# Optimization experiments

Measured on AMD Instinct MI355X. Metric: run time of the kernel, lower is better.

## Reference

```python
import jax, jax.numpy as jnp
import numpy as np
from jax import lax

NEG = -1e30  # safe -inf surrogate (avoids nan grads)
CTC_WEIGHT = 0.3


def _excl_cumsum(e):
    # exclusive cumsum along last axis: (..., U) -> (..., U+1)
    c = jnp.cumsum(e, axis=-1)
    return jnp.concatenate([jnp.zeros_like(c[..., :1]), c], axis=-1)


def _rnnt_loss(log_probs, targets, frame_len, tgt_len, blank):
    """RNNT forward DP. log_probs: (B,T,U+1,V) log-softmaxed. Returns per-seq NLL (B,)."""
    B, T, U1, V = log_probs.shape
    blank_lp = log_probs[..., blank]  # (B,T,U1)
    emit = jnp.take_along_axis(log_probs[:, :, :U1 - 1, :],
                               targets[:, None, :, None], axis=3)[..., 0]  # (B,T,U)
    # alpha[0,u] = sum_{j<u} emit[0,j]
    alpha0 = _excl_cumsum(emit[:, 0])  # (B,U1)

    def step(alpha_prev, inp):
        blank_prev, emit_t = inp  # (B,U1), (B,U)
        a = alpha_prev + blank_prev
        # alpha[t,u] = LSE(a_u, alpha[t,u-1] + emit[t,u-1]) solved in closed form:
        # alpha[t,u] = E[u] + cumLSE_{k<=u}(a_k - E[k]),  E = exclusive cumsum of emit
        E = _excl_cumsum(emit_t)
        alpha_t = E + lax.associative_scan(jnp.logaddexp, a - E, axis=-1)
        return alpha_t, alpha_t

    xs = (jnp.swapaxes(blank_lp[:, :-1], 0, 1), jnp.swapaxes(emit[:, 1:], 0, 1))
    _, alphas = lax.scan(step, alpha0, xs)
    alphas = jnp.concatenate([alpha0[None], alphas], axis=0)  # (T,B,U1)
    bi = jnp.arange(B)
    t_idx = frame_len - 1
    ll = alphas[t_idx, bi, tgt_len] + blank_lp[bi, t_idx, tgt_len]
    return -ll


def _ctc_loss(log_probs, targets, frame_len, tgt_len, blank):
    """CTC forward DP. log_probs: (B,T,V) log-softmaxed. Returns per-seq NLL (B,)."""
    B, T, V = log_probs.shape
    U = targets.shape[1]
    S = 2 * U + 1
    ext = jnp.full((B, S), blank, dtype=targets.dtype).at[:, 1::2].set(targets)  # (B,S)
    lp_ext = jnp.take_along_axis(log_probs, ext[:, None, :], axis=2)  # (B,T,S)
    ext_m2 = jnp.pad(ext[:, :-2], ((0, 0), (2, 0)), constant_values=blank)
    can_skip = (jnp.arange(S)[None, :] >= 2) & (ext != blank) & (ext != ext_m2)
    alpha0 = jnp.full((B, S), NEG).at[:, 0].set(lp_ext[:, 0, 0]).at[:, 1].set(lp_ext[:, 0, 1])

    def step(alpha, lp_t):
        p1 = jnp.pad(alpha[:, :-1], ((0, 0), (1, 0)), constant_values=NEG)
        p2 = jnp.where(can_skip,
                       jnp.pad(alpha[:, :-2], ((0, 0), (2, 0)), constant_values=NEG), NEG)
        m = jnp.maximum(jnp.maximum(alpha, p1), p2)
        new = lp_t + m + jnp.log(jnp.exp(alpha - m) + jnp.exp(p1 - m) + jnp.exp(p2 - m))
        return new, new

    _, alphas = lax.scan(step, alpha0, jnp.swapaxes(lp_ext, 0, 1)[1:])
    alphas = jnp.concatenate([alpha0[None], alphas], axis=0)  # (T,B,S)
    bi = jnp.arange(B)
    t_idx = frame_len - 1
    a_last = alphas[t_idx, bi, 2 * tgt_len]
    a_prev = alphas[t_idx, bi, 2 * tgt_len - 1]
    return -jnp.logaddexp(a_last, a_prev)


def setup_inputs() -> dict:
    key = jax.random.key(0)
    ks = jax.random.split(key, 9)
    B, T, U, V = 4, 200, 50, 1024
    D, H = 512, 640
    return {
        "x_enc": jax.random.normal(ks[0], (B, T, D), jnp.float32),
        "x_dec": jax.random.normal(ks[1], (B, U + 1, H), jnp.float32),
        "target": jax.random.randint(ks[2], (B, U), 0, V - 1),  # excludes blank = V-1
        "frame_length": jax.random.randint(ks[3], (B,), 150, T + 1).astype(jnp.int32),
        "target_length": jax.random.randint(ks[4], (B,), 30, U + 1).astype(jnp.int32),
        "W_ctc": jax.random.normal(ks[5], (D, V), jnp.float32) * 0.02,
        "b_ctc": jnp.zeros((V,), jnp.float32),
        "W_enc": jax.random.normal(ks[6], (D, H), jnp.float32) * 0.02,
        "W_pred": jax.random.normal(ks[7], (H, H), jnp.float32) * 0.02,
        "b_joint": jnp.zeros((H,), jnp.float32),
        "W_out": jax.random.normal(ks[8], (H, V), jnp.float32) * 0.02,
        "b_out": jnp.zeros((V,), jnp.float32),
    }


def reference(x_enc, x_dec, target, frame_length, target_length,
              W_ctc, b_ctc, W_enc, W_pred, b_joint, W_out, b_out):
    B = x_enc.shape[0]
    V = W_ctc.shape[1]
    blank = V - 1
    # CTC head: linear + log_softmax over vocab
    ctc_lp = jax.nn.log_softmax(x_enc @ W_ctc + b_ctc, axis=-1)  # (B,T,V)
    # Joiner: enc proj (B,T,1,J) + pred proj (B,1,U+1,J) -> tanh -> vocab
    joint = jnp.tanh(jnp.einsum('btd,dj->btj', x_enc, W_enc)[:, :, None, :]
                     + jnp.einsum('buh,hj->buj', x_dec, W_pred)[:, None, :, :]
                     + b_joint)  # (B,T,U+1,J)
    rnnt_lp = jax.nn.log_softmax(jnp.einsum('btuj,jv->btuv', joint, W_out) + b_out, axis=-1)
    rnnt = _rnnt_loss(rnnt_lp, target, frame_length, target_length, blank).mean()
    ctc = _ctc_loss(ctc_lp, target, frame_length, target_length, blank).sum() / B
    return rnnt + CTC_WEIGHT * ctc
```

## Files before the change

kernel.cpp:

```cpp
#include <hip/hip_runtime.h>
#include <hip/hip_bf16.h>

typedef __bf16 bf16_t;
typedef __attribute__((ext_vector_type(8))) __bf16 bf16x8;
typedef __attribute__((ext_vector_type(4))) float f32x4;
typedef __attribute__((ext_vector_type(2))) long long2_t;

#define NEGV (-1e30f)

#define BB 4
#define TT 200
#define UU 50
#define U1 51
#define VV 1024
#define DD 512
#define HH 640
#define RTOT (BB*TT*U1)
#define RPAD 40832
#define SS 101

__device__ __forceinline__ float lae(float a, float b) {
    float mx = fmaxf(a, b);
    return mx + __logf(__expf(a - mx) + __expf(b - mx));
}
__device__ __forceinline__ float lae3(float a, float b, float c) {
    float mx = fmaxf(fmaxf(a, b), c);
    return mx + __logf(__expf(a - mx) + __expf(b - mx) + __expf(c - mx));
}
__device__ __forceinline__ float tanh_fast(float x) {
    float ex = __expf(2.f * x);
    return 1.f - 2.f / (ex + 1.f);
}

__device__ __forceinline__ void pack_seg(const float* __restrict__ W, bf16_t* __restrict__ Wf,
                                         int e, int K32, int N)
{
    int j  = e & 7;
    int l  = (e >> 3) & 63;
    int kk = (e >> 9) % K32;
    int nt = e / (K32 * 512);
    int v = nt * 16 + (l & 15);
    int k = kk * 32 + ((l >> 4) << 2) + (j & 3) + ((j >> 2) << 4);
    Wf[e] = (bf16_t)W[(size_t)k * N + v];
}

__device__ __forceinline__ void pack_out8(const float* __restrict__ W, unsigned* __restrict__ Wf8,
                                          int e32)
{
    int word = e32 & 3;
    int l    = (e32 >> 2) & 63;
    int kkp  = (e32 >> 8) % 10;
    int nt   = e32 / 2560;
    int v  = nt * 16 + (l & 15);
    int kk = kkp * 2 + (word >> 1);
    int jb = (word & 1) * 4;
    float f[4];
#pragma unroll
    for (int t = 0; t < 4; ++t) {
        int j = jb + t;
        int k = kk * 32 + ((l >> 4) << 2) + (j & 3) + ((j >> 2) << 4);
        f[t] = W[(size_t)k * VV + v] * 16.f;
    }
    unsigned r = __builtin_amdgcn_cvt_pk_fp8_f32(f[0], f[1], 0, false);
    r = __builtin_amdgcn_cvt_pk_fp8_f32(f[2], f[3], r, true);
    Wf8[e32] = r;
}

__global__ void pack_all(const float* __restrict__ Wout, const float* __restrict__ Wenc,
                         const float* __restrict__ Wpred, const float* __restrict__ Wctc,
                         unsigned* __restrict__ FOut8, bf16_t* __restrict__ FEnc,
                         bf16_t* __restrict__ FPred, bf16_t* __restrict__ FCtc)
{
    int e = blockIdx.x * 256 + threadIdx.x;
    if (e < 163840) { pack_out8(Wout, FOut8, e); return; }
    e -= 163840;
    if (e < 327680) { pack_seg(Wenc, FEnc, e, 16, 640); return; }
    e -= 327680;
    if (e < 409600) { pack_seg(Wpred, FPred, e, 20, 640); return; }
    e -= 409600;
    pack_seg(Wctc, FCtc, e, 16, 1024);
}

template<int K32, int L, bool LSE, int J>
__device__ void gemm_dev(const float* __restrict__ A, int M, int rowbase, int K,
                         const bf16_t* __restrict__ Wf, const float* __restrict__ bias,
                         float* __restrict__ C, float* __restrict__ lse_out, int N,
                         bf16_t* Atile, float (*ps)[8])
{
    const int tid = threadIdx.x;
#pragma unroll
    for (int it = 0; it < J * K32 / 8; ++it) {
        int fi = it * 512 + tid;
        int l = fi & 63, jk = fi >> 6;
        int j = jk / K32, kk = jk - j * K32;
        int row = rowbase + j * 16 + (l & 15);
        if (row > M - 1) row = M - 1;
        int c0 = kk * 32 + ((l >> 4) << 2);
        const float4 a0 = *(const float4*)&A[(size_t)row * K + c0];
        const float4 a1 = *(const float4*)&A[(size_t)row * K + c0 + 16];
        bf16x8 v;
        v[0] = (bf16_t)a0.x; v[1] = (bf16_t)a0.y; v[2] = (bf16_t)a0.z; v[3] = (bf16_t)a0.w;
        v[4] = (bf16_t)a1.x; v[5] = (bf16_t)a1.y; v[6] = (bf16_t)a1.z; v[7] = (bf16_t)a1.w;
        *(bf16x8*)&Atile[(size_t)fi * 8] = v;
    }
    __syncthreads();

    const int l = tid & 63, w = tid >> 6;
    const int lrow = l & 15, lhi = l >> 4;

    f32x4 acc[J][L];
#pragma unroll
    for (int j = 0; j < J; ++j)
#pragma unroll
        for (int li = 0; li < L; ++li) acc[j][li] = f32x4{0.f, 0.f, 0.f, 0.f};

    for (int kk = 0; kk < K32; ++kk) {
        bf16x8 a[J];
#pragma unroll
        for (int j = 0; j < J; ++j)
            a[j] = *(const bf16x8*)&Atile[(size_t)(((j * K32 + kk) * 64 + l) * 8)];
#pragma unroll
        for (int li = 0; li < L; ++li) {
            bf16x8 b = *(const bf16x8*)&Wf[(size_t)(((w * L + li) * K32 + kk) * 64 + l) * 8];
#pragma unroll
            for (int j = 0; j < J; ++j)
                acc[j][li] = __builtin_amdgcn_mfma_f32_16x16x32_bf16(a[j], b, acc[j][li], 0, 0, 0);
        }
    }

    float se[J][4];
    if (LSE) {
#pragma unroll
        for (int j = 0; j < J; ++j)
#pragma unroll
            for (int i = 0; i < 4; ++i) se[j][i] = 0.f;
    }
#pragma unroll
    for (int j = 0; j < J; ++j)
#pragma unroll
        for (int li = 0; li < L; ++li) {
            int col = (w * L + li) * 16 + lrow;
            float bv = bias ? bias[col] : 0.f;
#pragma unroll
            for (int i = 0; i < 4; ++i) {
                int grow = rowbase + 16 * j + lhi * 4 + i;
                float x = acc[j][li][i] + bv;
                if (grow < M) C[(size_t)grow * N + col] = x;
                if (LSE) se[j][i] += __expf(x);
            }
        }
    if (LSE) {
#pragma unroll
        for (int d = 1; d < 16; d <<= 1)
#pragma unroll
            for (int j = 0; j < J; ++j)
#pragma unroll
                for (int i = 0; i < 4; ++i) se[j][i] += __shfl_xor(se[j][i], d);
        if (lrow == 0) {
#pragma unroll
            for (int j = 0; j < J; ++j)
#pragma unroll
                for (int i = 0; i < 4; ++i) ps[16 * j + lhi * 4 + i][w] = se[j][i];
        }
        __syncthreads();
        if (tid < J * 16) {
            float s = 0.f;
#pragma unroll
            for (int w0 = 0; w0 < 8; ++w0) s += ps[tid][w0];
            int grow = rowbase + tid;
            if (grow < M) lse_out[grow] = __logf(s);
        }
    }
}

__global__ __launch_bounds__(512)
void mfma_gemm3(const float* __restrict__ x_enc, const float* __restrict__ x_dec,
                const bf16_t* __restrict__ FEnc, const bf16_t* __restrict__ FPred,
                const bf16_t* __restrict__ FCtc, const float* __restrict__ b_ctc,
                float* __restrict__ enc_proj, float* __restrict__ pred_proj,
                float* __restrict__ ctc_logits, float* __restrict__ ctc_lse)
{
    __shared__ bf16_t Atile[40960];
    __shared__ float ps[64][8];
    int blk = blockIdx.x;
    if (blk < 13)
        gemm_dev<16, 5, false, 4>(x_enc, 800, blk * 64, 512, FEnc, nullptr, enc_proj, nullptr, 640, Atile, ps);
    else if (blk < 17)
        gemm_dev<20, 5, false, 4>(x_dec, 204, (blk - 13) * 64, 640, FPred, nullptr, pred_proj, nullptr, 640, Atile, ps);
    else
        gemm_dev<16, 8, true, 4>(x_enc, 800, (blk - 17) * 64, 512, FCtc, b_ctc, ctc_logits, ctc_lse, 1024, Atile, ps);
}

__global__ __launch_bounds__(512)
void joint_gemm(const float* __restrict__ enc,
                const float* __restrict__ pred,
                const float* __restrict__ bj,
                const unsigned* __restrict__ Wf8,
                const float* __restrict__ bo,
                const int* __restrict__ target,
                float* __restrict__ blank_buf, float* __restrict__ emit_buf)
{
    __shared__ __align__(16) char smbuf[40960];
    char* Afrag8 = smbuf;
    const int tid = threadIdx.x;
    const int blk = blockIdx.x;

    const int l = tid & 63, w = tid >> 6;
    const int lrow = l & 15, lhi = l >> 4;

#pragma unroll
    for (int it = 0; it < 5; ++it) {
        int c = it * 512 + tid;
        int ll = c & 63, jk = c >> 6;
        int j = jk / 10, kkp = jk - j * 10;
        int row = j * 16 + (ll & 15);
        int r = blk * 64 + row; if (r > RTOT - 1) r = RTOT - 1;
        int b = r / (TT * U1); int rem = r - b * (TT * U1);
        int t = rem / U1;      int u = rem - t * U1;
        const float* erow = enc + (size_t)(b * TT + t) * HH;
        const float* prow = pred + (size_t)(b * U1 + u) * HH;
        int cb = kkp * 64 + ((ll >> 4) << 2);
        float f[16];
#pragma unroll
        for (int s = 0; s < 4; ++s) {
            int off = cb + s * 16;
            const float4 e4 = *(const float4*)&erow[off];
            const float4 p4 = *(const float4*)&prow[off];
            const float4 q4 = *(const float4*)&bj[off];
            f[s * 4 + 0] = tanh_fast(e4.x + p4.x + q4.x);
            f[s * 4 + 1] = tanh_fast(e4.y + p4.y + q4.y);
            f[s * 4 + 2] = tanh_fast(e4.z + p4.z + q4.z);
            f[s * 4 + 3] = tanh_fast(e4.w + p4.w + q4.w);
        }
        uint4 v;
        unsigned r0 = __builtin_amdgcn_cvt_pk_fp8_f32(f[0], f[1], 0, false);
        v.x = __builtin_amdgcn_cvt_pk_fp8_f32(f[2], f[3], r0, true);
        r0 = __builtin_amdgcn_cvt_pk_fp8_f32(f[4], f[5], 0, false);
        v.y = __builtin_amdgcn_cvt_pk_fp8_f32(f[6], f[7], r0, true);
        r0 = __builtin_amdgcn_cvt_pk_fp8_f32(f[8], f[9], 0, false);
        v.z = __builtin_amdgcn_cvt_pk_fp8_f32(f[10], f[11], r0, true);
        r0 = __builtin_amdgcn_cvt_pk_fp8_f32(f[12], f[13], 0, false);
        v.w = __builtin_amdgcn_cvt_pk_fp8_f32(f[14], f[15], r0, true);
        *(uint4*)&Afrag8[(size_t)c * 16] = v;
    }
    __syncthreads();

    f32x4 acc[4][8];
#pragma unroll
    for (int j = 0; j < 4; ++j)
#pragma unroll
        for (int li = 0; li < 8; ++li) acc[j][li] = f32x4{0.f, 0.f, 0.f, 0.f};

    const char* Bp8 = (const char*)Wf8 + (size_t)(w * 8) * 10240 + (size_t)l * 16;

    const int rot = blk % 10;
    auto kstep = [&](int kkp) {
        long2_t a[4];
#pragma unroll
        for (int j = 0; j < 4; ++j)
            a[j] = *(const long2_t*)&Afrag8[(size_t)(((j * 10 + kkp) * 64 + l) * 16)];
#pragma unroll
        for (int li = 0; li < 8; ++li) {
            long2_t b = *(const long2_t*)(Bp8 + (size_t)li * 10240 + (size_t)kkp * 1024);
#pragma unroll
            for (int j = 0; j < 4; ++j)
                acc[j][li] = __builtin_amdgcn_mfma_f32_16x16x32_fp8_fp8(a[j][0], b[0], acc[j][li], 0, 0, 0);
#pragma unroll
            for (int j = 0; j < 4; ++j)
                acc[j][li] = __builtin_amdgcn_mfma_f32_16x16x32_fp8_fp8(a[j][1], b[1], acc[j][li], 0, 0, 0);
        }
    };
    for (int kkp = rot; kkp < 10; ++kkp) kstep(kkp);
    for (int kkp = 0; kkp < rot; ++kkp) kstep(kkp);

    int tg[4][4];
#pragma unroll
    for (int j = 0; j < 4; ++j)
#pragma unroll
        for (int i = 0; i < 4; ++i) {
            int r = blk * 64 + 16 * j + lhi * 4 + i; if (r > RTOT - 1) r = RTOT - 1;
            int b = r / (TT * U1); int rem = r - b * (TT * U1);
            int u = rem % U1;
            tg[j][i] = (u < UU) ? target[b * UU + u] : -1;
        }

    float se[4][4], ee[4][4], bbv[4][4];
#pragma unroll
    for (int j = 0; j < 4; ++j)
#pragma unroll
        for (int i = 0; i < 4; ++i) { se[j][i] = 0.f; ee[j][i] = NEGV; bbv[j][i] = NEGV; }

#pragma unroll
    for (int li = 0; li < 8; ++li) {
        int col = (w * 8 + li) * 16 + lrow;
        float bv = bo[col];
#pragma unroll
        for (int j = 0; j < 4; ++j)
#pragma unroll
            for (int i = 0; i < 4; ++i) {
                float x = acc[j][li][i] * 0.0625f + bv;
                se[j][i] += __expf(x);
                if (col == tg[j][i]) ee[j][i] = x;
            }
    }
    if (w == 7) {
        float bv = bo[1023];
#pragma unroll
        for (int j = 0; j < 4; ++j)
#pragma unroll
            for (int i = 0; i < 4; ++i) {
                float x = acc[j][7][i] * 0.0625f + bv;
                if (lrow == 15) bbv[j][i] = x;
            }
    }
#pragma unroll
    for (int d = 1; d < 16; d <<= 1)
#pragma unroll
        for (int j = 0; j < 4; ++j)
#pragma unroll
            for (int i = 0; i < 4; ++i) {
                se[j][i] += __shfl_xor(se[j][i], d);
                ee[j][i] = fmaxf(ee[j][i], __shfl_xor(ee[j][i], d));
                bbv[j][i] = fmaxf(bbv[j][i], __shfl_xor(bbv[j][i], d));
            }

    __syncthreads();
    float (*ps)[8] = (float (*)[8])(smbuf);
    float (*pe)[8] = (float (*)[8])(smbuf + 2048);
    float (*pb)[8] = (float (*)[8])(smbuf + 4096);
    if (lrow == 0) {
#pragma unroll
        for (int j = 0; j < 4; ++j)
#pragma unroll
            for (int i = 0; i < 4; ++i) {
                int r = 16 * j + lhi * 4 + i;
                ps[r][w] = se[j][i]; pe[r][w] = ee[j][i]; pb[r][w] = bbv[j][i];
            }
    }
    __syncthreads();
    if (tid < 64) {
        float s = 0.f, e = NEGV, bq = NEGV;
#pragma unroll
        for (int w0 = 0; w0 < 8; ++w0) {
            s += ps[tid][w0];
            e = fmaxf(e, pe[tid][w0]);
            bq = fmaxf(bq, pb[tid][w0]);
        }
        float lse = __logf(s);
        int gid = blk * 64 + tid;
        if (gid < RTOT) {
            blank_buf[gid] = bq - lse;
            emit_buf[gid]  = e - lse;
        }
    }
}

__global__ __launch_bounds__(256)
void dp_fused(const float* __restrict__ blank_buf, const float* __restrict__ emit_buf,
              const float* __restrict__ ctc_logits, const float* __restrict__ ctc_lse,
              const int* __restrict__ target, const int* __restrict__ frame_len,
              const int* __restrict__ tgt_len,
              float* __restrict__ loss_rnnt, float* __restrict__ loss_ctc)
{
    __shared__ __align__(16) float sm[28416];
    const int bid = blockIdx.x;
    const int tid = threadIdx.x;

    if (bid < 4) {
        const int b = bid;
        float2* pk = (float2*)sm;
        for (int i = tid; i < TT * U1; i += 256) {
            int t = i / U1, uu = i - t * U1;
            float bl = blank_buf[(b * TT + t) * U1 + uu];
            float em = emit_buf[(b * TT + t) * U1 + uu];
            pk[uu * 217 + t + 8] = make_float2(bl, em);
        }
        __syncthreads();
        if (tid >= 64) return;
        const int u = tid;
        const int fl = frame_len[b], tl = tgt_len[b];
        const int dh = fl - 1 + tl;
        const bool isTL = (u == tl);
        const bool act = (u < U1);
        float A = (u == 0) ? 0.f : NEGV;
        float Asave = (dh == 0 && isTL) ? A : NEGV;
        const float2* prow = pk + u * 217;

        for (int d0 = 1; d0 <= 249; d0 += 8) {
            int tb = d0 - 1 - u;
            int tc = tb; if (tc < -8) tc = -8; if (tc > 200) tc = 200;
            float2 buf[8];
#pragma unroll
            for (int s = 0; s < 8; ++s) buf[s] = prow[tc + 8 + s];
#pragma unroll
            for (int s = 0; s < 8; ++s) {
                int d = d0 + s;
                int t_new = d - u;
                float2 be = buf[s];
                float vshare = A + be.y;
                float left = __shfl_up(vshare, 1);
                if (u == 0) left = NEGV;
                float up = (t_new >= 1) ? (A + be.x) : NEGV;
                float Anew = lae(up, left);
                bool valid = act && (t_new >= 0) && (t_new < TT);
                A = valid ? Anew : A;
                Asave = (isTL && d == dh) ? A : Asave;
            }
        }
        if (isTL && act) {
            float bl = prow[(fl - 1) + 8].x;
            loss_rnnt[b] = -(Asave + bl);
        }
    } else {
        const int b = bid - 4;
        float* lpE = sm;
        float* lpO = sm + 208;
        for (int i = tid; i < TT; i += 256) {
            int bt = b * TT + i;
            lpE[i] = ctc_logits[(size_t)bt * VV + (VV - 1)] - ctc_lse[bt];
        }
        for (int i = tid; i < TT * UU; i += 256) {
            int t = i / UU, uu = i - t * UU;
            int bt = b * TT + t;
            lpO[uu * 209 + t] = ctc_logits[(size_t)bt * VV + target[b * UU + uu]] - ctc_lse[bt];
        }
        __syncthreads();
        if (tid >= 64) return;
        const int u = tid;
        const int fl = frame_len[b], tl = tgt_len[b];
        const bool acte = (u <= 50);
        const bool acto = (u < 50);
        bool skip = (u >= 1 && u < UU) ? (target[b * UU + u] != target[b * UU + u - 1]) : false;
        const float* orow = lpO + u * 209;
        float old_e = (u == 0) ? lpE[0] : NEGV;
        float old_o = (u == 0) ? orow[0] : NEGV;
        float Esave = (fl == 1) ? old_e : NEGV;
        float Osave = (fl == 1) ? old_o : NEGV;

        for (int t0 = 1; t0 <= 193; t0 += 8) {
            float bo8[8], be8[8];
#pragma unroll
            for (int s = 0; s < 8; ++s) { bo8[s] = orow[t0 + s]; be8[s] = lpE[t0 + s]; }
#pragma unroll
            for (int s = 0; s < 8; ++s) {
                int t = t0 + s;
                float prev_o = __shfl_up(old_o, 1);
                if (u == 0) prev_o = NEGV;
                float ne = be8[s] + lae(old_e, prev_o);
                float no = bo8[s] + lae3(old_o, old_e, skip ? prev_o : NEGV);
                old_e = acte ? ne : NEGV;
                old_o = acto ? no : NEGV;
                bool hv = (t == fl - 1) && (t < TT);
                Esave = hv ? old_e : Esave;
                Osave = hv ? old_o : Osave;
            }
        }
        float a_last = __shfl(Esave, tl);
        float a_prev = __shfl(Osave, tl - 1);
        if (u == 0) loss_ctc[b] = -lae(a_last, a_prev);
    }
}

__global__ void combine(const float* __restrict__ lr, const float* __restrict__ lc,
                        float* __restrict__ out)
{
    float r = 0.25f * (lr[0] + lr[1] + lr[2] + lr[3]);
    float c = 0.25f * (lc[0] + lc[1] + lc[2] + lc[3]);
    out[0] = r + 0.3f * c;
}

extern "C" void kernel_launch(void* const* d_in, const int* in_sizes, int n_in,
                              void* d_out, int out_size, void* d_ws, size_t ws_size,
                              hipStream_t stream)
{
    const float* x_enc   = (const float*)d_in[0];
    const float* x_dec   = (const float*)d_in[1];
    const int*   target  = (const int*)d_in[2];
    const int*   frame_l = (const int*)d_in[3];
    const int*   tgt_l   = (const int*)d_in[4];
    const float* W_ctc   = (const float*)d_in[5];
    const float* b_ctc   = (const float*)d_in[6];
    const float* W_enc   = (const float*)d_in[7];
    const float* W_pred  = (const float*)d_in[8];
    const float* b_joint = (const float*)d_in[9];
    const float* W_out   = (const float*)d_in[10];
    const float* b_out   = (const float*)d_in[11];
    float* out = (float*)d_out;

    float* wsf        = (float*)d_ws;
    float* enc_proj   = wsf;
    float* pred_proj  = wsf + 512000;
    float* ctc_logits = wsf + 642560;
    float* ctc_lse    = wsf + 1461760;
    float* blank_buf  = wsf + 1462592;
    float* emit_buf   = wsf + 1503424;
    float* loss_rnnt  = wsf + 1544256;
    float* loss_ctc   = wsf + 1544260;
    unsigned* FOut8 = (unsigned*)(wsf + 1544272);
    bf16_t* FEnc  = (bf16_t*)(wsf + 1708112);
    bf16_t* FPred = (bf16_t*)(wsf + 1871952);
    bf16_t* FCtc  = (bf16_t*)(wsf + 2076752);

    pack_all<<<5568, 256, 0, stream>>>(W_out, W_enc, W_pred, W_ctc, FOut8, FEnc, FPred, FCtc);
    mfma_gemm3<<<30, 512, 0, stream>>>(x_enc, x_dec, FEnc, FPred, FCtc, b_ctc,
                                       enc_proj, pred_proj, ctc_logits, ctc_lse);
    joint_gemm<<<RPAD / 64, 512, 0, stream>>>(enc_proj, pred_proj, b_joint, FOut8, b_out,
                                              target, blank_buf, emit_buf);
    dp_fused<<<8, 256, 0, stream>>>(blank_buf, emit_buf, ctc_logits, ctc_lse,
                                    target, frame_l, tgt_l, loss_rnnt, loss_ctc);
    combine<<<1, 1, 0, stream>>>(loss_rnnt, loss_ctc, out);
}
```

Measured before the change: 166.2 us.

## Retile joint GEMM to 128-row blocks split across vocab halves

The joint GEMM now gives each block 128 rows and half of the vocabulary instead of 64 rows and the full vocabulary. Each half writes partial softmax sums and max logits, and the DP kernel merges them into log-softmax blank and emit values. The tanh/fp8 A-tile is built twice, once per half, and LDS use doubles to 80KB, which may lower occupancy. The smaller projection GEMMs are also split into 32-row blocks so 57 blocks run instead of 30, giving more parallelism.

```diff
diff --git a/kernel.cpp b/kernel.cpp
--- a/kernel.cpp
+++ b/kernel.cpp
@@ -16,7 +16,6 @@
 #define DD 512
 #define HH 640
 #define RTOT (BB*TT*U1)
-#define RPAD 40832
 #define SS 101
 
 __device__ __forceinline__ float lae(float a, float b) {
@@ -180,15 +179,15 @@
                 float* __restrict__ enc_proj, float* __restrict__ pred_proj,
                 float* __restrict__ ctc_logits, float* __restrict__ ctc_lse)
 {
-    __shared__ bf16_t Atile[40960];
-    __shared__ float ps[64][8];
+    __shared__ bf16_t Atile[20480];
+    __shared__ float ps[32][8];
     int blk = blockIdx.x;
-    if (blk < 13)
-        gemm_dev<16, 5, false, 4>(x_enc, 800, blk * 64, 512, FEnc, nullptr, enc_proj, nullptr, 640, Atile, ps);
-    else if (blk < 17)
-        gemm_dev<20, 5, false, 4>(x_dec, 204, (blk - 13) * 64, 640, FPred, nullptr, pred_proj, nullptr, 640, Atile, ps);
+    if (blk < 25)
+        gemm_dev<16, 5, false, 2>(x_enc, 800, blk * 32, 512, FEnc, nullptr, enc_proj, nullptr, 640, Atile, ps);
+    else if (blk < 32)
+        gemm_dev<20, 5, false, 2>(x_dec, 204, (blk - 25) * 32, 640, FPred, nullptr, pred_proj, nullptr, 640, Atile, ps);
     else
-        gemm_dev<16, 8, true, 4>(x_enc, 800, (blk - 17) * 64, 512, FCtc, b_ctc, ctc_logits, ctc_lse, 1024, Atile, ps);
+        gemm_dev<16, 8, true, 2>(x_enc, 800, (blk - 32) * 32, 512, FCtc, b_ctc, ctc_logits, ctc_lse, 1024, Atile, ps);
 }
 
 __global__ __launch_bounds__(512)
@@ -198,23 +197,27 @@
                 const unsigned* __restrict__ Wf8,
                 const float* __restrict__ bo,
                 const int* __restrict__ target,
-                float* __restrict__ blank_buf, float* __restrict__ emit_buf)
-{
-    __shared__ __align__(16) char smbuf[40960];
+                float* __restrict__ psum0, float* __restrict__ psum1,
+                float* __restrict__ pee0, float* __restrict__ pee1,
+                float* __restrict__ pbb)
+{
+    __shared__ __align__(16) char smbuf[81920];
     char* Afrag8 = smbuf;
     const int tid = threadIdx.x;
     const int blk = blockIdx.x;
+    const int blk_row = blk >> 1;
+    const int half = blk & 1;
 
     const int l = tid & 63, w = tid >> 6;
     const int lrow = l & 15, lhi = l >> 4;
 
 #pragma unroll
-    for (int it = 0; it < 5; ++it) {
+    for (int it = 0; it < 10; ++it) {
         int c = it * 512 + tid;
         int ll = c & 63, jk = c >> 6;
         int j = jk / 10, kkp = jk - j * 10;
         int row = j * 16 + (ll & 15);
-        int r = blk * 64 + row; if (r > RTOT - 1) r = RTOT - 1;
+        int r = blk_row * 128 + row; if (r > RTOT - 1) r = RTOT - 1;
         int b = r / (TT * U1); int rem = r - b * (TT * U1);
         int t = rem / U1;      int u = rem - t * U1;
         const float* erow = enc + (size_t)(b * TT + t) * HH;
@@ -245,100 +248,89 @@
     }
     __syncthreads();
 
-    f32x4 acc[4][8];
-#pragma unroll
-    for (int j = 0; j < 4; ++j)
-#pragma unroll
-        for (int li = 0; li < 8; ++li) acc[j][li] = f32x4{0.f, 0.f, 0.f, 0.f};
-
-    const char* Bp8 = (const char*)Wf8 + (size_t)(w * 8) * 10240 + (size_t)l * 16;
+    f32x4 acc[8][4];
+#pragma unroll
+    for (int j = 0; j < 8; ++j)
+#pragma unroll
+        for (int li = 0; li < 4; ++li) acc[j][li] = f32x4{0.f, 0.f, 0.f, 0.f};
+
+    const char* Bp8 = (const char*)Wf8 + (size_t)(half * 32 + w * 4) * 10240 + (size_t)l * 16;
 
     const int rot = blk % 10;
     auto kstep = [&](int kkp) {
-        long2_t a[4];
-#pragma unroll
-        for (int j = 0; j < 4; ++j)
+        long2_t a[8];
+#pragma unroll
+        for (int j = 0; j < 8; ++j)
             a[j] = *(const long2_t*)&Afrag8[(size_t)(((j * 10 + kkp) * 64 + l) * 16)];
 #pragma unroll
-        for (int li = 0; li < 8; ++li) {
+        for (int li = 0; li < 4; ++li) {
             long2_t b = *(const long2_t*)(Bp8 + (size_t)li * 10240 + (size_t)kkp * 1024);
 #pragma unroll
-            for (int j = 0; j < 4; ++j)
+            for (int j = 0; j < 8; ++j)
                 acc[j][li] = __builtin_amdgcn_mfma_f32_16x16x32_fp8_fp8(a[j][0], b[0], acc[j][li], 0, 0, 0);
 #pragma unroll
-            for (int j = 0; j < 4; ++j)
+            for (int j = 0; j < 8; ++j)
                 acc[j][li] = __builtin_amdgcn_mfma_f32_16x16x32_fp8_fp8(a[j][1], b[1], acc[j][li], 0, 0, 0);
         }
     };
     for (int kkp = rot; kkp < 10; ++kkp) kstep(kkp);
     for (int kkp = 0; kkp < rot; ++kkp) kstep(kkp);
 
-    int tg[4][4];
-#pragma unroll
-    for (int j = 0; j < 4; ++j)
+    __syncthreads();
+    float (*ps)[8] = (float (*)[8])(smbuf);
+    float (*pe)[8] = (float (*)[8])(smbuf + 4096);
+    float (*pb)[8] = (float (*)[8])(smbuf + 8192);
+
+#pragma unroll
+    for (int j = 0; j < 8; ++j) {
+        int tg[4];
 #pragma unroll
         for (int i = 0; i < 4; ++i) {
-            int r = blk * 64 + 16 * j + lhi * 4 + i; if (r > RTOT - 1) r = RTOT - 1;
+            int r = blk_row * 128 + 16 * j + lhi * 4 + i; if (r > RTOT - 1) r = RTOT - 1;
             int b = r / (TT * U1); int rem = r - b * (TT * U1);
             int u = rem % U1;
-            tg[j][i] = (u < UU) ? target[b * UU + u] : -1;
-        }
-
-    float se[4][4], ee[4][4], bbv[4][4];
-#pragma unroll
-    for (int j = 0; j < 4; ++j)
-#pragma unroll
-        for (int i = 0; i < 4; ++i) { se[j][i] = 0.f; ee[j][i] = NEGV; bbv[j][i] = NEGV; }
-
-#pragma unroll
-    for (int li = 0; li < 8; ++li) {
-        int col = (w * 8 + li) * 16 + lrow;
-        float bv = bo[col];
-#pragma unroll
-        for (int j = 0; j < 4; ++j)
+            tg[i] = (u < UU) ? target[b * UU + u] : -1;
+        }
+        float se[4], ee[4], bb4[4];
+#pragma unroll
+        for (int i = 0; i < 4; ++i) { se[i] = 0.f; ee[i] = NEGV; bb4[i] = NEGV; }
+#pragma unroll
+        for (int li = 0; li < 4; ++li) {
+            int col = (half * 32 + w * 4 + li) * 16 + lrow;
+            float bv = bo[col];
 #pragma unroll
             for (int i = 0; i < 4; ++i) {
                 float x = acc[j][li][i] * 0.0625f + bv;
-                se[j][i] += __expf(x);
-                if (col == tg[j][i]) ee[j][i] = x;
-            }
-    }
-    if (w == 7) {
-        float bv = bo[1023];
-#pragma unroll
-        for (int j = 0; j < 4; ++j)
+                se[i] += __expf(x);
+                if (col == tg[i]) ee[i] = x;
+            }
+        }
+        if (half == 1 && w == 7) {
+            float bv = bo[1023];
 #pragma unroll
             for (int i = 0; i < 4; ++i) {
-                float x = acc[j][7][i] * 0.0625f + bv;
-                if (lrow == 15) bbv[j][i] = x;
-            }
-    }
-#pragma unroll
-    for (int d = 1; d < 16; d <<= 1)
-#pragma unroll
-        for (int j = 0; j < 4; ++j)
+                float x = acc[j][3][i] * 0.0625f + bv;
+                if (lrow == 15) bb4[i] = x;
+            }
+        }
+#pragma unroll
+        for (int d = 1; d < 16; d <<= 1)
 #pragma unroll
             for (int i = 0; i < 4; ++i) {
-                se[j][i] += __shfl_xor(se[j][i], d);
-                ee[j][i] = fmaxf(ee[j][i], __shfl_xor(ee[j][i], d));
-                bbv[j][i] = fmaxf(bbv[j][i], __shfl_xor(bbv[j][i], d));
-            }
-
+                se[i] += __shfl_xor(se[i], d);
+                ee[i] = fmaxf(ee[i], __shfl_xor(ee[i], d));
+                bb4[i] = fmaxf(bb4[i], __shfl_xor(bb4[i], d));
+            }
+        if (lrow == 0) {
+#pragma unroll
+            for (int i = 0; i < 4; ++i) {
+                int rr = 16 * j + lhi * 4 + i;
+                ps[rr][w] = se[i]; pe[rr][w] = ee[i]; pb[rr][w] = bb4[i];
+            }
+        }
+    }
     __syncthreads();
-    float (*ps)[8] = (float (*)[8])(smbuf);
-    float (*pe)[8] = (float (*)[8])(smbuf + 2048);
-    float (*pb)[8] = (float (*)[8])(smbuf + 4096);
-    if (lrow == 0) {
-#pragma unroll
-        for (int j = 0; j < 4; ++j)
-#pragma unroll
-            for (int i = 0; i < 4; ++i) {
-                int r = 16 * j + lhi * 4 + i;
-                ps[r][w] = se[j][i]; pe[r][w] = ee[j][i]; pb[r][w] = bbv[j][i];
-            }
-    }
-    __syncthreads();
-    if (tid < 64) {
+    if (tid < 128) {
         float s = 0.f, e = NEGV, bq = NEGV;
 #pragma unroll
         for (int w0 = 0; w0 < 8; ++w0) {
@@ -346,17 +338,18 @@
             e = fmaxf(e, pe[tid][w0]);
             bq = fmaxf(bq, pb[tid][w0]);
         }
-        float lse = __logf(s);
-        int gid = blk * 64 + tid;
+        int gid = blk_row * 128 + tid;
         if (gid < RTOT) {
-            blank_buf[gid] = bq - lse;
-            emit_buf[gid]  = e - lse;
+            if (half == 0) { psum0[gid] = s; pee0[gid] = e; }
+            else           { psum1[gid] = s; pee1[gid] = e; pbb[gid] = bq; }
         }
     }
 }
 
 __global__ __launch_bounds__(256)
-void dp_fused(const float* __restrict__ blank_buf, const float* __restrict__ emit_buf,
+void dp_fused(const float* __restrict__ psum0, const float* __restrict__ psum1,
+              const float* __restrict__ pee0, const float* __restrict__ pee1,
+              const float* __restrict__ pbb,
               const float* __restrict__ ctc_logits, const float* __restrict__ ctc_lse,
               const int* __restrict__ target, const int* __restrict__ frame_len,
               const int* __restrict__ tgt_len,
@@ -371,8 +364,11 @@
         float2* pk = (float2*)sm;
         for (int i = tid; i < TT * U1; i += 256) {
             int t = i / U1, uu = i - t * U1;
-            float bl = blank_buf[(b * TT + t) * U1 + uu];
-            float em = emit_buf[(b * TT + t) * U1 + uu];
+            int r = b * (TT * U1) + i;
+            float s = psum0[r] + psum1[r];
+            float lse = __logf(s);
+            float bl = pbb[r] - lse;
+            float em = fmaxf(pee0[r], pee1[r]) - lse;
             pk[uu * 217 + t + 8] = make_float2(bl, em);
         }
         __syncthreads();
@@ -492,21 +488,25 @@
     float* pred_proj  = wsf + 512000;
     float* ctc_logits = wsf + 642560;
     float* ctc_lse    = wsf + 1461760;
-    float* blank_buf  = wsf + 1462592;
-    float* emit_buf   = wsf + 1503424;
-    float* loss_rnnt  = wsf + 1544256;
-    float* loss_ctc   = wsf + 1544260;
-    unsigned* FOut8 = (unsigned*)(wsf + 1544272);
-    bf16_t* FEnc  = (bf16_t*)(wsf + 1708112);
-    bf16_t* FPred = (bf16_t*)(wsf + 1871952);
-    bf16_t* FCtc  = (bf16_t*)(wsf + 2076752);
+    float* psum0      = wsf + 1462592;
+    float* psum1      = wsf + 1503552;
+    float* pee0       = wsf + 1544512;
+    float* pee1       = wsf + 1585472;
+    float* pbb        = wsf + 1626432;
+    float* loss_rnnt  = wsf + 1667392;
+    float* loss_ctc   = wsf + 1667396;
+    unsigned* FOut8 = (unsigned*)(wsf + 1667408);
+    bf16_t* FEnc  = (bf16_t*)(wsf + 1831248);
+    bf16_t* FPred = (bf16_t*)(wsf + 1995088);
+    bf16_t* FCtc  = (bf16_t*)(wsf + 2199888);
 
     pack_all<<<5568, 256, 0, stream>>>(W_out, W_enc, W_pred, W_ctc, FOut8, FEnc, FPred, FCtc);
-    mfma_gemm3<<<30, 512, 0, stream>>>(x_enc, x_dec, FEnc, FPred, FCtc, b_ctc,
+    mfma_gemm3<<<57, 512, 0, stream>>>(x_enc, x_dec, FEnc, FPred, FCtc, b_ctc,
                                        enc_proj, pred_proj, ctc_logits, ctc_lse);
-    joint_gemm<<<RPAD / 64, 512, 0, stream>>>(enc_proj, pred_proj, b_joint, FOut8, b_out,
-                                              target, blank_buf, emit_buf);
-    dp_fused<<<8, 256, 0, stream>>>(blank_buf, emit_buf, ctc_logits, ctc_lse,
+    joint_gemm<<<638, 512, 0, stream>>>(enc_proj, pred_proj, b_joint, FOut8, b_out,
+                                        target, psum0, psum1, pee0, pee1, pbb);
+    dp_fused<<<8, 256, 0, stream>>>(psum0, psum1, pee0, pee1, pbb,
+                                    ctc_logits, ctc_lse,
                                     target, frame_l, tgt_l, loss_rnnt, loss_ctc);
     combine<<<1, 1, 0, stream>>>(loss_rnnt, loss_ctc, out);
 }
```

After: 212.8 us. +28.0%, slower.

## Split joint GEMM vocab across two blocks and move W_out packing into gemm3

Applied to the files above, without the earlier changes.

The joint GEMM now launches two 256-thread blocks per 64-row tile, each covering half of the vocabulary. Each block writes partial softmax sums and partial emit/blank maxima, and the DP kernel merges them into log-probs. The FP8 packing of W_out moves out of the bf16 pack kernel into extra blocks of the projection GEMM kernel, so it can overlap with the small GEMMs. The aim is more blocks and better occupancy for the dominant joint GEMM, at the cost of building the tanh/fp8 A tile twice and extra global partial buffers.

```diff
diff --git a/kernel.cpp b/kernel.cpp
--- a/kernel.cpp
+++ b/kernel.cpp
@@ -16,7 +16,6 @@
 #define DD 512
 #define HH 640
 #define RTOT (BB*TT*U1)
-#define RPAD 40832
 #define SS 101
 
 __device__ __forceinline__ float lae(float a, float b) {
@@ -66,14 +65,12 @@
     Wf8[e32] = r;
 }
 
-__global__ void pack_all(const float* __restrict__ Wout, const float* __restrict__ Wenc,
-                         const float* __restrict__ Wpred, const float* __restrict__ Wctc,
-                         unsigned* __restrict__ FOut8, bf16_t* __restrict__ FEnc,
-                         bf16_t* __restrict__ FPred, bf16_t* __restrict__ FCtc)
+__global__ void pack_bf16(const float* __restrict__ Wenc, const float* __restrict__ Wpred,
+                          const float* __restrict__ Wctc,
+                          bf16_t* __restrict__ FEnc, bf16_t* __restrict__ FPred,
+                          bf16_t* __restrict__ FCtc)
 {
     int e = blockIdx.x * 256 + threadIdx.x;
-    if (e < 163840) { pack_out8(Wout, FOut8, e); return; }
-    e -= 163840;
     if (e < 327680) { pack_seg(Wenc, FEnc, e, 16, 640); return; }
     e -= 327680;
     if (e < 409600) { pack_seg(Wpred, FPred, e, 20, 640); return; }
@@ -178,11 +175,17 @@
                 const bf16_t* __restrict__ FEnc, const bf16_t* __restrict__ FPred,
                 const bf16_t* __restrict__ FCtc, const float* __restrict__ b_ctc,
                 float* __restrict__ enc_proj, float* __restrict__ pred_proj,
-                float* __restrict__ ctc_logits, float* __restrict__ ctc_lse)
+                float* __restrict__ ctc_logits, float* __restrict__ ctc_lse,
+                const float* __restrict__ Wout, unsigned* __restrict__ FOut8)
 {
     __shared__ bf16_t Atile[40960];
     __shared__ float ps[64][8];
     int blk = blockIdx.x;
+    if (blk >= 30) {
+        int e = (blk - 30) * 512 + threadIdx.x;
+        pack_out8(Wout, FOut8, e);
+        return;
+    }
     if (blk < 13)
         gemm_dev<16, 5, false, 4>(x_enc, 800, blk * 64, 512, FEnc, nullptr, enc_proj, nullptr, 640, Atile, ps);
     else if (blk < 17)
@@ -191,30 +194,35 @@
         gemm_dev<16, 8, true, 4>(x_enc, 800, (blk - 17) * 64, 512, FCtc, b_ctc, ctc_logits, ctc_lse, 1024, Atile, ps);
 }
 
-__global__ __launch_bounds__(512)
+__global__ __launch_bounds__(256)
 void joint_gemm(const float* __restrict__ enc,
                 const float* __restrict__ pred,
                 const float* __restrict__ bj,
                 const unsigned* __restrict__ Wf8,
                 const float* __restrict__ bo,
                 const int* __restrict__ target,
-                float* __restrict__ blank_buf, float* __restrict__ emit_buf)
+                float* __restrict__ psum0, float* __restrict__ psum1,
+                float* __restrict__ pee0, float* __restrict__ pee1,
+                float* __restrict__ pbb)
 {
     __shared__ __align__(16) char smbuf[40960];
+    __shared__ float ps[64][4], pe[64][4], pb[64][4];
     char* Afrag8 = smbuf;
     const int tid = threadIdx.x;
     const int blk = blockIdx.x;
+    const int blk_row = blk >> 1;
+    const int half = blk & 1;
 
     const int l = tid & 63, w = tid >> 6;
     const int lrow = l & 15, lhi = l >> 4;
 
 #pragma unroll
-    for (int it = 0; it < 5; ++it) {
-        int c = it * 512 + tid;
+    for (int it = 0; it < 10; ++it) {
+        int c = it * 256 + tid;
         int ll = c & 63, jk = c >> 6;
         int j = jk / 10, kkp = jk - j * 10;
         int row = j * 16 + (ll & 15);
-        int r = blk * 64 + row; if (r > RTOT - 1) r = RTOT - 1;
+        int r = blk_row * 64 + row; if (r > RTOT - 1) r = RTOT - 1;
         int b = r / (TT * U1); int rem = r - b * (TT * U1);
         int t = rem / U1;      int u = rem - t * U1;
         const float* erow = enc + (size_t)(b * TT + t) * HH;
@@ -251,7 +259,7 @@
 #pragma unroll
         for (int li = 0; li < 8; ++li) acc[j][li] = f32x4{0.f, 0.f, 0.f, 0.f};
 
-    const char* Bp8 = (const char*)Wf8 + (size_t)(w * 8) * 10240 + (size_t)l * 16;
+    const char* Bp8 = (const char*)Wf8 + (size_t)(half * 32 + w * 8) * 10240 + (size_t)l * 16;
 
     const int rot = blk % 10;
     auto kstep = [&](int kkp) {
@@ -278,7 +286,7 @@
     for (int j = 0; j < 4; ++j)
 #pragma unroll
         for (int i = 0; i < 4; ++i) {
-            int r = blk * 64 + 16 * j + lhi * 4 + i; if (r > RTOT - 1) r = RTOT - 1;
+            int r = blk_row * 64 + 16 * j + lhi * 4 + i; if (r > RTOT - 1) r = RTOT - 1;
             int b = r / (TT * U1); int rem = r - b * (TT * U1);
             int u = rem % U1;
             tg[j][i] = (u < UU) ? target[b * UU + u] : -1;
@@ -292,7 +300,7 @@
 
 #pragma unroll
     for (int li = 0; li < 8; ++li) {
-        int col = (w * 8 + li) * 16 + lrow;
+        int col = (half * 32 + w * 8 + li) * 16 + lrow;
         float bv = bo[col];
 #pragma unroll
         for (int j = 0; j < 4; ++j)
@@ -303,7 +311,7 @@
                 if (col == tg[j][i]) ee[j][i] = x;
             }
     }
-    if (w == 7) {
+    if (half == 1 && w == 3) {
         float bv = bo[1023];
 #pragma unroll
         for (int j = 0; j < 4; ++j)
@@ -323,11 +331,6 @@
                 ee[j][i] = fmaxf(ee[j][i], __shfl_xor(ee[j][i], d));
                 bbv[j][i] = fmaxf(bbv[j][i], __shfl_xor(bbv[j][i], d));
             }
-
-    __syncthreads();
-    float (*ps)[8] = (float (*)[8])(smbuf);
-    float (*pe)[8] = (float (*)[8])(smbuf + 2048);
-    float (*pb)[8] = (float (*)[8])(smbuf + 4096);
     if (lrow == 0) {
 #pragma unroll
         for (int j = 0; j < 4; ++j)
@@ -341,22 +344,23 @@
     if (tid < 64) {
         float s = 0.f, e = NEGV, bq = NEGV;
 #pragma unroll
-        for (int w0 = 0; w0 < 8; ++w0) {
+        for (int w0 = 0; w0 < 4; ++w0) {
             s += ps[tid][w0];
             e = fmaxf(e, pe[tid][w0]);
             bq = fmaxf(bq, pb[tid][w0]);
         }
-        float lse = __logf(s);
-        int gid = blk * 64 + tid;
+        int gid = blk_row * 64 + tid;
         if (gid < RTOT) {
-            blank_buf[gid] = bq - lse;
-            emit_buf[gid]  = e - lse;
+            if (half == 0) { psum0[gid] = s; pee0[gid] = e; }
+            else           { psum1[gid] = s; pee1[gid] = e; pbb[gid] = bq; }
         }
     }
 }
 
 __global__ __launch_bounds__(256)
-void dp_fused(const float* __restrict__ blank_buf, const float* __restrict__ emit_buf,
+void dp_fused(const float* __restrict__ psum0, const float* __restrict__ psum1,
+              const float* __restrict__ pee0, const float* __restrict__ pee1,
+              const float* __restrict__ pbb,
               const float* __restrict__ ctc_logits, const float* __restrict__ ctc_lse,
               const int* __restrict__ target, const int* __restrict__ frame_len,
               const int* __restrict__ tgt_len,
@@ -371,8 +375,11 @@
         float2* pk = (float2*)sm;
         for (int i = tid; i < TT * U1; i += 256) {
             int t = i / U1, uu = i - t * U1;
-            float bl = blank_buf[(b * TT + t) * U1 + uu];
-            float em = emit_buf[(b * TT + t) * U1 + uu];
+            int r = b * (TT * U1) + i;
+            float s = psum0[r] + psum1[r];
+            float lse = __logf(s);
+            float bl = pbb[r] - lse;
+            float em = fmaxf(pee0[r], pee1[r]) - lse;
             pk[uu * 217 + t + 8] = make_float2(bl, em);
         }
         __syncthreads();
@@ -492,21 +499,26 @@
     float* pred_proj  = wsf + 512000;
     float* ctc_logits = wsf + 642560;
     float* ctc_lse    = wsf + 1461760;
-    float* blank_buf  = wsf + 1462592;
-    float* emit_buf   = wsf + 1503424;
-    float* loss_rnnt  = wsf + 1544256;
-    float* loss_ctc   = wsf + 1544260;
-    unsigned* FOut8 = (unsigned*)(wsf + 1544272);
-    bf16_t* FEnc  = (bf16_t*)(wsf + 1708112);
-    bf16_t* FPred = (bf16_t*)(wsf + 1871952);
-    bf16_t* FCtc  = (bf16_t*)(wsf + 2076752);
-
-    pack_all<<<5568, 256, 0, stream>>>(W_out, W_enc, W_pred, W_ctc, FOut8, FEnc, FPred, FCtc);
-    mfma_gemm3<<<30, 512, 0, stream>>>(x_enc, x_dec, FEnc, FPred, FCtc, b_ctc,
-                                       enc_proj, pred_proj, ctc_logits, ctc_lse);
-    joint_gemm<<<RPAD / 64, 512, 0, stream>>>(enc_proj, pred_proj, b_joint, FOut8, b_out,
-                                              target, blank_buf, emit_buf);
-    dp_fused<<<8, 256, 0, stream>>>(blank_buf, emit_buf, ctc_logits, ctc_lse,
+    float* psum0      = wsf + 1462592;
+    float* psum1      = wsf + 1503552;
+    float* pee0       = wsf + 1544512;
+    float* pee1       = wsf + 1585472;
+    float* pbb        = wsf + 1626432;
+    float* loss_rnnt  = wsf + 1667392;
+    float* loss_ctc   = wsf + 1667396;
+    unsigned* FOut8 = (unsigned*)(wsf + 1667408);
+    bf16_t* FEnc  = (bf16_t*)(wsf + 1831248);
+    bf16_t* FPred = (bf16_t*)(wsf + 1995088);
+    bf16_t* FCtc  = (bf16_t*)(wsf + 2199888);
+
+    pack_bf16<<<4928, 256, 0, stream>>>(W_enc, W_pred, W_ctc, FEnc, FPred, FCtc);
+    mfma_gemm3<<<350, 512, 0, stream>>>(x_enc, x_dec, FEnc, FPred, FCtc, b_ctc,
+                                        enc_proj, pred_proj, ctc_logits, ctc_lse,
+                                        W_out, FOut8);
+    joint_gemm<<<1276, 256, 0, stream>>>(enc_proj, pred_proj, b_joint, FOut8, b_out,
+                                         target, psum0, psum1, pee0, pee1, pbb);
+    dp_fused<<<8, 256, 0, stream>>>(psum0, psum1, pee0, pee1, pbb,
+                                    ctc_logits, ctc_lse,
                                     target, frame_l, tgt_l, loss_rnnt, loss_ctc);
     combine<<<1, 1, 0, stream>>>(loss_rnnt, loss_ctc, out);
 }
```

Measured after the change: 231.5 us. 1.39x slower.
